# Kernel tuning notes

Hardware: AMD Instinct MI355X
Metric: run time of the kernel (lower is better)

## Reference

```python
import jax, jax.numpy as jnp
import numpy as np

B, S, I, H = 64, 2048, 512, 512


def setup_inputs() -> dict:
    key = jax.random.key(0)
    k1, k2, k3 = jax.random.split(key, 3)
    x_enc = jax.random.normal(k1, (B, S, I), dtype=jnp.float32)
    # Packed gate weights: columns = [i | f | o | c | d], scaled like typical init
    W = jax.random.normal(k2, (I + H, 5 * H), dtype=jnp.float32) * (1.0 / np.sqrt(I + H))
    b = jax.random.normal(k3, (5 * H,), dtype=jnp.float32) * 0.01
    return {"x_enc": x_enc, "W": W, "b": b}


def reference(x_enc, W, b):
    Bb, Ss, Ii = x_enc.shape
    Hh = W.shape[1] // 5

    def step(carry, x_t):
        h, c = carry
        z = jnp.concatenate([x_t, h], axis=-1) @ W + b  # [B, 5H]
        zi, zf, zo, zc, zd = jnp.split(z, 5, axis=-1)
        i_t = jax.nn.sigmoid(zi)
        f_t = jax.nn.sigmoid(zf)
        o_t = jax.nn.sigmoid(zo)
        c_prime = f_t * c + i_t * jnp.tanh(zc)
        d_t = jnp.tanh(zd)
        c_new = c_prime + d_t * (c_prime - c)  # highway-style update
        h_new = o_t * jnp.tanh(c_new)
        return (h_new, c_new), h_new

    h0 = jnp.zeros((Bb, Hh), dtype=x_enc.dtype)
    c0 = jnp.zeros((Bb, Hh), dtype=x_enc.dtype)
    xs = jnp.transpose(x_enc, (1, 0, 2))  # [S, B, I]
    _, ys = jax.lax.scan(step, (h0, c0), xs)
    return jnp.transpose(ys, (1, 0, 2))  # [B, S, H]
```

## Files before the change

kernel.cpp:

```cpp
#include <hip/hip_runtime.h>
#include <stdint.h>


typedef _Float16 h8 __attribute__((ext_vector_type(8)));
typedef _Float16 h4v __attribute__((ext_vector_type(4)));
typedef float f4 __attribute__((ext_vector_type(4)));

#define SCOPE_AGENT __HIP_MEMORY_SCOPE_AGENT

__device__ __forceinline__ float sigf(float x) {
  x = fminf(fmaxf(x, -40.f), 40.f);
  return 1.f / (1.f + __expf(-x));
}
__device__ __forceinline__ float tanh_f(float x) {
  x = fminf(fmaxf(x, -20.f), 20.f);
  const float e = __expf(2.f * x);
  return (e - 1.f) / (e + 1.f);
}

__global__ __launch_bounds__(256) void k_wt(const float* __restrict__ W,
                                            _Float16* __restrict__ Wt) {
  __shared__ __align__(16) _Float16 tl[64][68];
  const int bk = blockIdx.x & 15;
  const int bn = blockIdx.x >> 4;
  const int t = threadIdx.x;
  {
    const int r = t >> 2, c4 = t & 3;
    const float4* s4 = (const float4*)(W + (size_t)(bk * 64 + r) * 2560 + bn * 64 + c4 * 16);
#pragma unroll
    for (int i = 0; i < 4; i++) {
      float4 v = s4[i];
      tl[r][c4 * 16 + i * 4 + 0] = (_Float16)v.x;
      tl[r][c4 * 16 + i * 4 + 1] = (_Float16)v.y;
      tl[r][c4 * 16 + i * 4 + 2] = (_Float16)v.z;
      tl[r][c4 * 16 + i * 4 + 3] = (_Float16)v.w;
    }
  }
  __syncthreads();
  {
    const int nr = t >> 2, kk = (t & 3) * 16;
    h8 o0, o1;
#pragma unroll
    for (int i = 0; i < 8; i++) {
      o0[i] = tl[kk + i][nr];
      o1[i] = tl[kk + 8 + i][nr];
    }
    _Float16* dst = Wt + (size_t)(bn * 64 + nr) * 1024 + bk * 64 + kk;
    *(h8*)dst = o0;
    *(h8*)(dst + 8) = o1;
  }
}

__global__ __launch_bounds__(256) void k_zx(const float* __restrict__ X,
                                            const _Float16* __restrict__ Wt,
                                            const float* __restrict__ bias,
                                            _Float16* __restrict__ Zx,
                                            int s_base, int CS) {
  __shared__ __align__(16) _Float16 As[128][72];
  __shared__ __align__(16) _Float16 Bs[128][72];
  const int bid = blockIdx.x;
  const int nblk = bid % 20;
  const int mblk = bid / 20;
  const int tilesPerB = CS >> 7;
  const int b = mblk / tilesPerB;
  const int s0 = (mblk - b * tilesPerB) << 7;
  const int t = threadIdx.x;
  const int wid = t >> 6, lane = t & 63;
  const int wr = wid >> 1, wc = wid & 1;
  const int lr = (lane >> 4) * 4, lc = lane & 15;
  const int koff = (lane >> 4) * 8;

  const f4 zero4 = {0.f, 0.f, 0.f, 0.f};
  f4 acc[4][4];
#pragma unroll
  for (int i = 0; i < 4; i++)
#pragma unroll
    for (int j = 0; j < 4; j++) acc[i][j] = zero4;

  const float* Xb = X + ((size_t)b * 2048 + (size_t)(s_base + s0)) * 512;
  const _Float16* Bb = Wt + (size_t)nblk * 128 * 1024;
  const int rA = t >> 1, hf = t & 1;

  for (int k0 = 0; k0 < 512; k0 += 64) {
    const float4* s4 = (const float4*)(Xb + (size_t)rA * 512 + k0 + hf * 32);
#pragma unroll
    for (int i = 0; i < 8; i++) {
      float4 v = s4[i];
      h4v o = {(_Float16)v.x, (_Float16)v.y, (_Float16)v.z, (_Float16)v.w};
      *(h4v*)&As[rA][hf * 32 + i * 4] = o;
    }
    const h8* bs = (const h8*)(Bb + (size_t)rA * 1024 + k0 + hf * 32);
#pragma unroll
    for (int i = 0; i < 4; i++) *(h8*)&Bs[rA][hf * 32 + i * 8] = bs[i];
    __syncthreads();
#pragma unroll
    for (int kk = 0; kk < 2; kk++) {
      h8 af[4], bf[4];
      const int kr = kk * 32 + koff;
#pragma unroll
      for (int i = 0; i < 4; i++) af[i] = *(const h8*)&As[wr * 64 + i * 16 + lc][kr];
#pragma unroll
      for (int j = 0; j < 4; j++) bf[j] = *(const h8*)&Bs[wc * 64 + j * 16 + lc][kr];
#pragma unroll
      for (int i = 0; i < 4; i++)
#pragma unroll
        for (int j = 0; j < 4; j++)
          acc[i][j] = __builtin_amdgcn_mfma_f32_16x16x32_f16(af[i], bf[j], acc[i][j], 0, 0, 0);
    }
    __syncthreads();
  }
#pragma unroll
  for (int j = 0; j < 4; j++) {
    const int col = nblk * 128 + wc * 64 + j * 16 + lc;
    const float bc = bias[col];
#pragma unroll
    for (int i = 0; i < 4; i++) {
#pragma unroll
      for (int r = 0; r < 4; r++) {
        const int srow = s0 + wr * 64 + i * 16 + lr + r;
        Zx[((size_t)b * CS + srow) * 2560 + col] = (_Float16)(acc[i][j][r] + bc);
      }
    }
  }
}

__global__ __launch_bounds__(256) void k_rec(
    const _Float16* __restrict__ Zx, const _Float16* __restrict__ Wt,
    float* __restrict__ Y, uint32_t* __restrict__ hbuf,
    _Float16* __restrict__ hstate, float* __restrict__ cstate,
    int s_base, int CS) {
  __shared__ __align__(16) _Float16 WsT[40][520];
  __shared__ __align__(16) _Float16 hs[16][520];
  __shared__ __align__(16) float zsh[16][40];
  __shared__ __align__(16) _Float16 zxs[16][40];
  __shared__ __align__(16) float cbuf[128];

  const int bid = blockIdx.x;
  const int grp = bid >> 6;
  const int ci = ((bid & 7) << 3) | ((bid >> 3) & 7);
  const int tid = threadIdx.x;
  const int wid = tid >> 6, lane = tid & 63;
  const int hbase = ci * 8;

#pragma unroll
  for (int i = 0; i < 10; i++) {
    const int idx = i * 256 + tid;
    const int lcw = idx >> 6;
    const int ch = idx & 63;
    const int g = lcw >> 3, j = lcw & 7;
    const h8* src = (const h8*)(Wt + (size_t)(g * 512 + hbase + j) * 1024 + 512 + ch * 8);
    *(h8*)&WsT[lcw][ch * 8] = *src;
  }
  if (tid < 128) {
    cbuf[tid] = cstate[(grp * 64 + ci) * 128 + tid];
    const int m = tid >> 3, j = tid & 7;
    _Float16 hv = hstate[(size_t)(grp * 16 + m) * 512 + hbase + j];
    uint16_t hb;
    __builtin_memcpy(&hb, &hv, 2);
    const uint32_t v = ((uint32_t)(s_base + 1) << 16) | (uint32_t)hb;
    __hip_atomic_store(&hbuf[((size_t)((s_base & 1) * 4 + grp) * 16 + m) * 512 + hbase + j],
                       v, __ATOMIC_RELAXED, SCOPE_AGENT);
  }
  __syncthreads();

  uint32_t* hs32 = (uint32_t*)&hs[0][0];

  for (int t = 0; t < CS; t++) {
    const int G = s_base + t;
    const uint32_t tag = (uint32_t)(G + 1);
    if (wid == 3) {
      for (int c = lane; c < 80; c += 64) {
        const int m = c / 5, g = c % 5;
        const h8* src =
            (const h8*)(Zx + ((size_t)(grp * 16 + m) * CS + t) * 2560 + g * 512 + hbase);
        *(h8*)&zxs[m][g * 8] = *src;
      }
    }
    {
      const uint64_t* src =
          (const uint64_t*)(hbuf + (size_t)((G & 1) * 4 + grp) * 16 * 512);
      uint64_t w[16];
#pragma unroll
      for (int i = 0; i < 16; i++)
        w[i] = __hip_atomic_load(&src[i * 256 + tid], __ATOMIC_RELAXED, SCOPE_AGENT);
#pragma unroll
      for (int i = 0; i < 16; i++) {
        while ((((uint32_t)w[i] >> 16) != tag) |
               (((uint32_t)(w[i] >> 48)) != tag))
          w[i] = __hip_atomic_load(&src[i * 256 + tid], __ATOMIC_RELAXED, SCOPE_AGENT);
        hs32[i * 260 + tid] =
            ((uint32_t)w[i] & 0xffffu) | (((uint32_t)(w[i] >> 32) & 0xffffu) << 16);
      }
    }
    __syncthreads();
    if (wid < 3) {
      f4 acc = {0.f, 0.f, 0.f, 0.f};
      const int nloc = wid * 16 + (lane & 15);
      const int wrow = nloc < 40 ? nloc : 39;
      const int koff = (lane >> 4) * 8;
#pragma unroll
      for (int ks = 0; ks < 16; ks++) {
        const h8 a = *(const h8*)&hs[lane & 15][ks * 32 + koff];
        const h8 bb = *(const h8*)&WsT[wrow][ks * 32 + koff];
        acc = __builtin_amdgcn_mfma_f32_16x16x32_f16(a, bb, acc, 0, 0, 0);
      }
      if (nloc < 40) {
        const int rb = (lane >> 4) * 4;
#pragma unroll
        for (int r = 0; r < 4; r++)
          zsh[rb + r][nloc] = acc[r] + (float)zxs[rb + r][nloc];
      }
    }
    __syncthreads();
    if (tid < 128) {
      const int m = tid >> 3, j = tid & 7;
      const float zi = zsh[m][j], zf = zsh[m][8 + j], zo = zsh[m][16 + j];
      const float zc = zsh[m][24 + j], zd = zsh[m][32 + j];
      const float ig = sigf(zi), fg = sigf(zf), og = sigf(zo);
      const float c0 = cbuf[tid];
      const float cp = fg * c0 + ig * tanh_f(zc);
      const float dg = tanh_f(zd);
      const float cn = cp + dg * (cp - c0);
      const float hv = og * tanh_f(cn);
      cbuf[tid] = cn;
      const _Float16 hfv = (_Float16)hv;
      uint16_t hb;
      __builtin_memcpy(&hb, &hfv, 2);
      const uint32_t v = ((uint32_t)(G + 2) << 16) | (uint32_t)hb;
      __hip_atomic_store(
          &hbuf[((size_t)(((G + 1) & 1) * 4 + grp) * 16 + m) * 512 + hbase + j], v,
          __ATOMIC_RELAXED, SCOPE_AGENT);
      asm volatile("" ::: "memory");
      Y[((size_t)(grp * 16 + m) * 2048 + (size_t)G) * 512 + hbase + j] = hv;
      if (t == CS - 1) {
        cstate[(grp * 64 + ci) * 128 + tid] = cn;
        hstate[(size_t)(grp * 16 + m) * 512 + hbase + j] = hfv;
      }
    }
  }
}

extern "C" void kernel_launch(void* const* d_in, const int* in_sizes, int n_in,
                              void* d_out, int out_size, void* d_ws, size_t ws_size,
                              hipStream_t stream) {
  const float* X = (const float*)d_in[0];
  const float* W = (const float*)d_in[1];
  const float* bias = (const float*)d_in[2];
  float* Y = (float*)d_out;
  char* ws = (char*)d_ws;

  const size_t szWt = (size_t)2560 * 1024 * 2;
  int CS = 128;
  for (int c = 2048; c >= 128; c >>= 1) {
    const size_t need = szWt + (size_t)64 * c * 2560 * 2 + 512 * 1024;
    if (need <= ws_size) { CS = c; break; }
  }
  const size_t offZx = szWt;
  const size_t szZx = (size_t)64 * CS * 2560 * 2;
  const size_t offHbuf = offZx + szZx;
  const size_t szHbuf = (size_t)2 * 4 * 16 * 512 * 4;
  const size_t offHst = offHbuf + szHbuf;
  const size_t szHst = (size_t)4 * 16 * 512 * 2;
  const size_t offCst = offHst + szHst;
  const size_t szCst = (size_t)4 * 64 * 128 * 4;

  _Float16* Wt = (_Float16*)(ws + 0);
  _Float16* Zx = (_Float16*)(ws + offZx);
  uint32_t* hbuf = (uint32_t*)(ws + offHbuf);
  _Float16* hstate = (_Float16*)(ws + offHst);
  float* cstate = (float*)(ws + offCst);

  k_wt<<<640, 256, 0, stream>>>(W, Wt);
  (void)hipMemsetAsync(ws + offHbuf, 0, szHbuf + szHst + szCst, stream);

  const int nch = 2048 / CS;
  for (int ch = 0; ch < nch; ch++) {
    const int sb = ch * CS;
    k_zx<<<CS * 10, 256, 0, stream>>>(X, Wt, bias, Zx, sb, CS);
    k_rec<<<256, 256, 0, stream>>>(Zx, Wt, Y, hbuf, hstate, cstate, sb, CS);
  }
  (void)in_sizes; (void)n_in; (void)out_size;
}
```

Measured before the change: 13.91 ms.

## Halve recurrent blocks, each owning 16 hidden units with 64-bit h stores

Each recurrent block now covers 16 hidden columns instead of 8, so 128 blocks run instead of 256, and all four waves share the MFMA work (wave 0 also computes a fifth tile). Each gate thread now handles two units and publishes two tagged h values with a single 64-bit atomic store and a float2 Y write. The Zx prefetch is spread across 160 threads and issued before the h spin-wait. The aim is to cut cross-block synchronisation traffic and per-step overhead, at the cost of more work per block and fewer CUs in use.

```diff
diff --git a/kernel.cpp b/kernel.cpp
--- a/kernel.cpp
+++ b/kernel.cpp
@@ -129,37 +129,38 @@
     float* __restrict__ Y, uint32_t* __restrict__ hbuf,
     _Float16* __restrict__ hstate, float* __restrict__ cstate,
     int s_base, int CS) {
-  __shared__ __align__(16) _Float16 WsT[40][520];
+  __shared__ __align__(16) _Float16 WsT[80][520];
   __shared__ __align__(16) _Float16 hs[16][520];
-  __shared__ __align__(16) float zsh[16][40];
-  __shared__ __align__(16) _Float16 zxs[16][40];
-  __shared__ __align__(16) float cbuf[128];
+  __shared__ __align__(16) float zsh[16][84];
+  __shared__ __align__(16) _Float16 zxs[16][80];
+  __shared__ __align__(16) float cbuf[256];
 
   const int bid = blockIdx.x;
-  const int grp = bid >> 6;
-  const int ci = ((bid & 7) << 3) | ((bid >> 3) & 7);
+  const int grp = bid >> 5;
+  const int ci = ((bid & 7) << 2) | ((bid >> 3) & 3);
   const int tid = threadIdx.x;
   const int wid = tid >> 6, lane = tid & 63;
-  const int hbase = ci * 8;
-
-#pragma unroll
-  for (int i = 0; i < 10; i++) {
+  const int hbase = ci * 16;
+
+#pragma unroll
+  for (int i = 0; i < 20; i++) {
     const int idx = i * 256 + tid;
     const int lcw = idx >> 6;
     const int ch = idx & 63;
-    const int g = lcw >> 3, j = lcw & 7;
-    const h8* src = (const h8*)(Wt + (size_t)(g * 512 + hbase + j) * 1024 + 512 + ch * 8);
+    const int g = lcw >> 4, jc = lcw & 15;
+    const h8* src = (const h8*)(Wt + (size_t)(g * 512 + hbase + jc) * 1024 + 512 + ch * 8);
     *(h8*)&WsT[lcw][ch * 8] = *src;
   }
+  cbuf[tid] = cstate[((size_t)(grp * 32 + ci)) * 256 + tid];
   if (tid < 128) {
-    cbuf[tid] = cstate[(grp * 64 + ci) * 128 + tid];
-    const int m = tid >> 3, j = tid & 7;
-    _Float16 hv = hstate[(size_t)(grp * 16 + m) * 512 + hbase + j];
-    uint16_t hb;
-    __builtin_memcpy(&hb, &hv, 2);
-    const uint32_t v = ((uint32_t)(s_base + 1) << 16) | (uint32_t)hb;
-    __hip_atomic_store(&hbuf[((size_t)((s_base & 1) * 4 + grp) * 16 + m) * 512 + hbase + j],
-                       v, __ATOMIC_RELAXED, SCOPE_AGENT);
+    const int m = tid >> 3, jj = (tid & 7) * 2;
+    uint32_t hv2;
+    __builtin_memcpy(&hv2, hstate + (size_t)(grp * 16 + m) * 512 + hbase + jj, 4);
+    const uint32_t tg = (uint32_t)(s_base + 1) << 16;
+    const uint64_t v = ((uint64_t)(tg | (hv2 >> 16)) << 32) | (tg | (hv2 & 0xffffu));
+    __hip_atomic_store(
+        (uint64_t*)&hbuf[((size_t)((s_base & 1) * 4 + grp) * 16 + m) * 512 + hbase + jj],
+        v, __ATOMIC_RELAXED, SCOPE_AGENT);
   }
   __syncthreads();
 
@@ -168,13 +169,11 @@
   for (int t = 0; t < CS; t++) {
     const int G = s_base + t;
     const uint32_t tag = (uint32_t)(G + 1);
-    if (wid == 3) {
-      for (int c = lane; c < 80; c += 64) {
-        const int m = c / 5, g = c % 5;
-        const h8* src =
-            (const h8*)(Zx + ((size_t)(grp * 16 + m) * CS + t) * 2560 + g * 512 + hbase);
-        *(h8*)&zxs[m][g * 8] = *src;
-      }
+    h8 zxr;
+    const int zm = tid / 10, zc8 = tid % 10;
+    if (tid < 160) {
+      zxr = *(const h8*)(Zx + ((size_t)(grp * 16 + zm) * CS + t) * 2560 +
+                         (zc8 >> 1) * 512 + hbase + (zc8 & 1) * 8);
     }
     {
       const uint64_t* src =
@@ -192,49 +191,69 @@
             ((uint32_t)w[i] & 0xffffu) | (((uint32_t)(w[i] >> 32) & 0xffffu) << 16);
       }
     }
+    if (tid < 160) *(h8*)&zxs[zm][zc8 * 8] = zxr;
     __syncthreads();
-    if (wid < 3) {
-      f4 acc = {0.f, 0.f, 0.f, 0.f};
-      const int nloc = wid * 16 + (lane & 15);
-      const int wrow = nloc < 40 ? nloc : 39;
-      const int koff = (lane >> 4) * 8;
-#pragma unroll
-      for (int ks = 0; ks < 16; ks++) {
-        const h8 a = *(const h8*)&hs[lane & 15][ks * 32 + koff];
-        const h8 bb = *(const h8*)&WsT[wrow][ks * 32 + koff];
-        acc = __builtin_amdgcn_mfma_f32_16x16x32_f16(a, bb, acc, 0, 0, 0);
-      }
-      if (nloc < 40) {
-        const int rb = (lane >> 4) * 4;
-#pragma unroll
-        for (int r = 0; r < 4; r++)
-          zsh[rb + r][nloc] = acc[r] + (float)zxs[rb + r][nloc];
+    {
+      const int cloc = lane & 15;
+      const int koffv = (lane >> 4) * 8;
+      const int rb = (lane >> 4) * 4;
+#pragma unroll
+      for (int rep = 0; rep < 2; rep++) {
+        if (rep == 0 || wid == 0) {
+          const int tl = (rep == 0) ? wid : 4;
+          f4 acc = {0.f, 0.f, 0.f, 0.f};
+#pragma unroll
+          for (int ks = 0; ks < 16; ks++) {
+            const h8 a = *(const h8*)&hs[cloc][ks * 32 + koffv];
+            const h8 b = *(const h8*)&WsT[tl * 16 + cloc][ks * 32 + koffv];
+            acc = __builtin_amdgcn_mfma_f32_16x16x32_f16(a, b, acc, 0, 0, 0);
+          }
+#pragma unroll
+          for (int r = 0; r < 4; r++)
+            zsh[rb + r][tl * 16 + cloc] = acc[r] + (float)zxs[rb + r][tl * 16 + cloc];
+        }
       }
     }
     __syncthreads();
     if (tid < 128) {
-      const int m = tid >> 3, j = tid & 7;
-      const float zi = zsh[m][j], zf = zsh[m][8 + j], zo = zsh[m][16 + j];
-      const float zc = zsh[m][24 + j], zd = zsh[m][32 + j];
-      const float ig = sigf(zi), fg = sigf(zf), og = sigf(zo);
-      const float c0 = cbuf[tid];
-      const float cp = fg * c0 + ig * tanh_f(zc);
-      const float dg = tanh_f(zd);
-      const float cn = cp + dg * (cp - c0);
-      const float hv = og * tanh_f(cn);
-      cbuf[tid] = cn;
-      const _Float16 hfv = (_Float16)hv;
-      uint16_t hb;
-      __builtin_memcpy(&hb, &hfv, 2);
-      const uint32_t v = ((uint32_t)(G + 2) << 16) | (uint32_t)hb;
+      const int m = tid >> 3, jj = (tid & 7) * 2;
+      float hv[2], cn2[2];
+#pragma unroll
+      for (int u = 0; u < 2; u++) {
+        const int j = jj + u;
+        const float zi = zsh[m][j];
+        const float zf = zsh[m][16 + j];
+        const float zo = zsh[m][32 + j];
+        const float zc = zsh[m][48 + j];
+        const float zd = zsh[m][64 + j];
+        const float ig = sigf(zi), fg = sigf(zf), og = sigf(zo);
+        const float c0 = cbuf[m * 16 + j];
+        const float cp = fg * c0 + ig * tanh_f(zc);
+        const float dg = tanh_f(zd);
+        const float cn = cp + dg * (cp - c0);
+        hv[u] = og * tanh_f(cn);
+        cn2[u] = cn;
+        cbuf[m * 16 + j] = cn;
+      }
+      _Float16 h0 = (_Float16)hv[0], h1 = (_Float16)hv[1];
+      uint16_t b0, b1;
+      __builtin_memcpy(&b0, &h0, 2);
+      __builtin_memcpy(&b1, &h1, 2);
+      const uint32_t tg = (uint32_t)(G + 2) << 16;
+      const uint64_t v = ((uint64_t)(tg | b1) << 32) | (tg | b0);
       __hip_atomic_store(
-          &hbuf[((size_t)(((G + 1) & 1) * 4 + grp) * 16 + m) * 512 + hbase + j], v,
-          __ATOMIC_RELAXED, SCOPE_AGENT);
+          (uint64_t*)&hbuf[((size_t)(((G + 1) & 1) * 4 + grp) * 16 + m) * 512 + hbase + jj],
+          v, __ATOMIC_RELAXED, SCOPE_AGENT);
       asm volatile("" ::: "memory");
-      Y[((size_t)(grp * 16 + m) * 2048 + (size_t)G) * 512 + hbase + j] = hv;
+      float2 yv;
+      yv.x = hv[0];
+      yv.y = hv[1];
+      *(float2*)&Y[((size_t)(grp * 16 + m) * 2048 + (size_t)G) * 512 + hbase + jj] = yv;
       if (t == CS - 1) {
-        cstate[(grp * 64 + ci) * 128 + tid] = cn;
-        hstate[(size_t)(grp * 16 + m) * 512 + hbase + j] = hfv;
+        cstate[((size_t)(grp * 32 + ci)) * 256 + m * 16 + jj] = cn2[0];
+        cstate[((size_t)(grp * 32 + ci)) * 256 + m * 16 + jj + 1] = cn2[1];
+        const uint32_t hh = ((uint32_t)b1 << 16) | b0;
+        __builtin_memcpy(hstate + (size_t)(grp * 16 + m) * 512 + hbase + jj, &hh, 4);
       }
     }
   }
@@ -262,7 +281,7 @@
   const size_t offHst = offHbuf + szHbuf;
   const size_t szHst = (size_t)4 * 16 * 512 * 2;
   const size_t offCst = offHst + szHst;
-  const size_t szCst = (size_t)4 * 64 * 128 * 4;
+  const size_t szCst = (size_t)4 * 32 * 256 * 4;
 
   _Float16* Wt = (_Float16*)(ws + 0);
   _Float16* Zx = (_Float16*)(ws + offZx);
@@ -277,7 +296,7 @@
   for (int ch = 0; ch < nch; ch++) {
     const int sb = ch * CS;
     k_zx<<<CS * 10, 256, 0, stream>>>(X, Wt, bias, Zx, sb, CS);
-    k_rec<<<256, 256, 0, stream>>>(Zx, Wt, Y, hbuf, hstate, cstate, sb, CS);
+    k_rec<<<128, 256, 0, stream>>>(Zx, Wt, Y, hbuf, hstate, cstate, sb, CS);
   }
   (void)in_sizes; (void)n_in; (void)out_size;
 }
```

New measurement: 15.14 ms. 8.8% more time.
